# Performance work log

Measured on AMD Instinct MI355X. Metric: run time of the kernel, lower is better.

## Reference

```python
import jax, jax.numpy as jnp
import numpy as np

N = 4096
IN_F = 256
OUT_F = 128
H = 2
ALPHA = 0.2  # leaky relu slope
NEG_INF = -9e15  # matches -9000000000000000.0 in the torch code


def setup_inputs() -> dict:
    key = jax.random.key(0)
    k_x, k_adj, k_w, k_a = jax.random.split(key, 4)
    x = jax.random.normal(k_x, (N, IN_F), dtype=jnp.float32)
    adj = (jax.random.uniform(k_adj, (N, N)) < 0.005).astype(jnp.float32)
    # xavier_uniform with gain=1.414 as in the torch module
    gain = 1.414
    bound_w = gain * np.sqrt(6.0 / (IN_F + OUT_F))
    W = jax.random.uniform(k_w, (H, IN_F, OUT_F), minval=-bound_w, maxval=bound_w, dtype=jnp.float32)
    bound_a = gain * np.sqrt(6.0 / (2 * OUT_F + 1))
    a = jax.random.uniform(k_a, (H, 2 * OUT_F, 1), minval=-bound_a, maxval=bound_a, dtype=jnp.float32)
    return {"x": x, "adj": adj, "W": W, "a": a}


def reference(x, adj, W, a):
    # Dense multi-head GAT layer (eval mode: dropout is identity).
    n = x.shape[0]
    h, _, f_out = W.shape
    adj = adj + jnp.eye(n, dtype=adj.dtype)  # add self loops
    xt = jnp.einsum('nf,hfo->hno', x, W)  # [H, N, F_out]
    # The repeat_interleave/repeat + concat + matmul(a) in the original is
    # exactly the additive decomposition: score[h,i,j] = xt[h,i]@a1[h] + xt[h,j]@a2[h]
    a1 = a[:, :f_out, 0]   # [H, F_out] (applied to target/query node i)
    a2 = a[:, f_out:, 0]   # [H, F_out] (applied to source node j)
    e1 = jnp.einsum('hno,ho->hn', xt, a1)  # [H, N]
    e2 = jnp.einsum('hno,ho->hn', xt, a2)  # [H, N]
    scores = jax.nn.leaky_relu(e1[:, :, None] + e2[:, None, :], negative_slope=ALPHA)  # [H,N,N]
    scores = jnp.where(adj > 0, scores, jnp.asarray(NEG_INF, scores.dtype))
    attn = jax.nn.softmax(scores, axis=-1)
    h_prime = jnp.einsum('hij,hjo->hio', attn, xt)  # [H, N, F_out]
    # concat=True branch: torch .view(N, H*F_out) on contiguous [H,N,F] -> same as reshape
    return jax.nn.elu(h_prime.reshape(n, h * f_out))
```

## Files before the change

### kernel.cpp

```cpp
#include <hip/hip_runtime.h>
#include <math.h>

#define IN_F 256
#define OUT_F 128
#define NHEAD 2
#define ALPHA 0.2f
#define NN 4096
#define NCAP 128

typedef __attribute__((ext_vector_type(8))) short short8;
typedef __attribute__((ext_vector_type(4))) float f32x4;
typedef const __attribute__((address_space(1))) void* gas_ptr;
typedef __attribute__((address_space(3))) void* las_ptr;

__device__ __forceinline__ void async_copy16(const void* g, void* l) {
  __builtin_amdgcn_global_load_lds((gas_ptr)g, (las_ptr)l, 16, 0, 0);
}

__device__ __forceinline__ ushort f2bf(float f) {
  unsigned u = __float_as_uint(f);
  u += 0x7fffu + ((u >> 16) & 1u);
  return (ushort)(u >> 16);
}

__device__ __forceinline__ float lrelu(float t) { return t > 0.f ? t : ALPHA * t; }

__global__ __launch_bounds__(256) void prep_w(
    const float* __restrict__ W, ushort* __restrict__ Wt) {
  int p = blockIdx.x * 256 + threadIdx.x;
  int h = p >> 13;
  int rem = p & 8191;
  int c = rem >> 7;
  int o = rem & 127;
  const float* wsrc = W + h * (IN_F * OUT_F) + (4 * c) * OUT_F + o;
  ushort4 ov;
  ov.x = f2bf(wsrc[0 * OUT_F]);
  ov.y = f2bf(wsrc[1 * OUT_F]);
  ov.z = f2bf(wsrc[2 * OUT_F]);
  ov.w = f2bf(wsrc[3 * OUT_F]);
  *(ushort4*)(Wt + ((size_t)h * OUT_F + o) * IN_F + 4 * c) = ov;
}

__global__ __launch_bounds__(256) void gemm_mfma(
    const float* __restrict__ x, const ushort* __restrict__ Wt,
    const float* __restrict__ a,
    float* __restrict__ xt, float* __restrict__ e1, float* __restrict__ e2) {
  __shared__ ushort sA[32 * 256];
  __shared__ ushort sB[128 * 256];
  __shared__ float sa[2 * OUT_F];
  __shared__ float se1[32], se2[32];

  const int h = blockIdx.y;
  const int rowBase = blockIdx.x * 32;
  const int tid = threadIdx.x;
  const int wave = tid >> 6, lane = tid & 63;
  const int wr = wave & 1, wc = wave >> 1;
  const int q = lane >> 4, l16 = lane & 15;
  const int ar = tid >> 3;
  const int ak = (tid & 7) * 8;

  const char* wbase = (const char*)(Wt + (size_t)h * (OUT_F * IN_F));
#pragma unroll
  for (int it = 0; it < 16; ++it) {
    int g = it * 256 + tid;
    int r = g >> 5, c32 = g & 31;
    async_copy16(wbase + r * 512 + ((c32 ^ (r & 7)) * 16),
                 (char*)sB + (size_t)(it * 256 + wave * 64) * 16);
  }

  const float* xrow = x + (size_t)(rowBase + ar) * IN_F + ak;
  float4 ax[8];
#pragma unroll
  for (int c = 0; c < 4; ++c) {
    ax[2 * c]     = *(const float4*)(xrow + 64 * c);
    ax[2 * c + 1] = *(const float4*)(xrow + 64 * c + 4);
  }
#pragma unroll
  for (int c = 0; c < 4; ++c) {
    float4 va = ax[2 * c], vb = ax[2 * c + 1];
    union { short8 s8; ushort u[8]; } pk;
    pk.u[0] = f2bf(va.x); pk.u[1] = f2bf(va.y);
    pk.u[2] = f2bf(va.z); pk.u[3] = f2bf(va.w);
    pk.u[4] = f2bf(vb.x); pk.u[5] = f2bf(vb.y);
    pk.u[6] = f2bf(vb.z); pk.u[7] = f2bf(vb.w);
    *(short8*)(sA + ar * 256 + ((ak + 64 * c) ^ ((ar & 7) << 3))) = pk.s8;
  }

  sa[tid] = a[h * (2 * OUT_F) + tid];

  f32x4 acc[4];
#pragma unroll
  for (int i = 0; i < 4; ++i) acc[i] = (f32x4)(0.0f);

  __syncthreads();

  const int arow = wr * 16 + l16;
  const int aswz = (arow & 7) << 3;
#pragma unroll
  for (int ks = 0; ks < 256; ks += 32) {
    short8 af = *(const short8*)(sA + arow * 256 + ((ks + q * 8) ^ aswz));
#pragma unroll
    for (int ct = 0; ct < 4; ++ct) {
      int col = wc * 64 + ct * 16 + l16;
      short8 bf = *(const short8*)(sB + col * 256 + ((ks + q * 8) ^ ((col & 7) << 3)));
      acc[ct] = __builtin_amdgcn_mfma_f32_16x16x32_bf16(af, bf, acc[ct], 0, 0, 0);
    }
  }

#pragma unroll
  for (int ct = 0; ct < 4; ++ct) {
    int col = wc * 64 + ct * 16 + l16;
#pragma unroll
    for (int reg = 0; reg < 4; ++reg) {
      int row = rowBase + wr * 16 + q * 4 + reg;
      xt[((size_t)h * NN + row) * OUT_F + col] = acc[ct][reg];
    }
  }

  float pe1[4], pe2[4];
#pragma unroll
  for (int reg = 0; reg < 4; ++reg) { pe1[reg] = 0.f; pe2[reg] = 0.f; }
#pragma unroll
  for (int ct = 0; ct < 4; ++ct) {
    int col = wc * 64 + ct * 16 + l16;
    float a1v = sa[col], a2v = sa[OUT_F + col];
#pragma unroll
    for (int reg = 0; reg < 4; ++reg) {
      pe1[reg] = fmaf(acc[ct][reg], a1v, pe1[reg]);
      pe2[reg] = fmaf(acc[ct][reg], a2v, pe2[reg]);
    }
  }
#pragma unroll
  for (int off = 1; off < 16; off <<= 1) {
#pragma unroll
    for (int reg = 0; reg < 4; ++reg) {
      pe1[reg] += __shfl_xor(pe1[reg], off, 64);
      pe2[reg] += __shfl_xor(pe2[reg], off, 64);
    }
  }
  if (wc == 0 && l16 == 0) {
#pragma unroll
    for (int reg = 0; reg < 4; ++reg) {
      int r = wr * 16 + q * 4 + reg;
      se1[r] = pe1[reg];
      se2[r] = pe2[reg];
    }
  }
  __syncthreads();
  if (wc == 1 && l16 == 0) {
#pragma unroll
    for (int reg = 0; reg < 4; ++reg) {
      int r = wr * 16 + q * 4 + reg;
      se1[r] += pe1[reg];
      se2[r] += pe2[reg];
    }
  }
  __syncthreads();
  if (tid < 32) {
    e1[(size_t)h * NN + rowBase + tid] = se1[tid];
    e2[(size_t)h * NN + rowBase + tid] = se2[tid];
  }
}

__global__ __launch_bounds__(256) void gat_aggregate(
    const float* __restrict__ adj, const float* __restrict__ xt,
    const float* __restrict__ e1, const float* __restrict__ e2,
    float* __restrict__ out) {
  __shared__ int s_nbr[4][NCAP];
  __shared__ float s_p0[4][NCAP];
  __shared__ float s_p1[4][NCAP];

  const int wave = threadIdx.x >> 6;
  const int lane = threadIdx.x & 63;
  const int i = blockIdx.x * 4 + wave;

  const float4* row4 = (const float4*)(adj + (size_t)i * NN);
  float4 v[16];
#pragma unroll
  for (int c = 0; c < 16; ++c) v[c] = row4[lane + c * 64];

  const unsigned long long lt = (1ull << lane) - 1ull;
  int cnt = 0;
#pragma unroll
  for (int c = 0; c < 16; ++c) {
    float vals[4] = {v[c].x, v[c].y, v[c].z, v[c].w};
#pragma unroll
    for (int s = 0; s < 4; ++s) {
      int j = (c * 64 + lane) * 4 + s;
      bool hit = (vals[s] > 0.f) || (j == i);
      unsigned long long mask = __ballot(hit);
      if (hit) {
        int pos = cnt + (int)__popcll(mask & lt);
        if (pos < NCAP) s_nbr[wave][pos] = j;
      }
      cnt += (int)__popcll(mask);
    }
  }
  const int m = cnt < NCAP ? cnt : NCAP;

  const float e10 = e1[i];
  const float e11 = e1[NN + i];
  float t0[2], t1[2];
  float mx0 = -3.0e38f, mx1 = -3.0e38f;
#pragma unroll
  for (int r = 0; r < 2; ++r) {
    int k = lane + r * 64;
    if (k < m) {
      int j = s_nbr[wave][k];
      t0[r] = lrelu(e10 + e2[j]);
      t1[r] = lrelu(e11 + e2[NN + j]);
      mx0 = fmaxf(mx0, t0[r]);
      mx1 = fmaxf(mx1, t1[r]);
    } else {
      t0[r] = -3.0e38f;
      t1[r] = -3.0e38f;
    }
  }
#pragma unroll
  for (int off = 32; off > 0; off >>= 1) {
    mx0 = fmaxf(mx0, __shfl_xor(mx0, off, 64));
    mx1 = fmaxf(mx1, __shfl_xor(mx1, off, 64));
  }

  float s0 = 0.f, s1 = 0.f;
#pragma unroll
  for (int r = 0; r < 2; ++r) {
    int k = lane + r * 64;
    if (k < m) {
      float p0 = __expf(t0[r] - mx0);
      float p1 = __expf(t1[r] - mx1);
      s_p0[wave][k] = p0;
      s_p1[wave][k] = p1;
      s0 += p0;
      s1 += p1;
    }
  }
#pragma unroll
  for (int off = 32; off > 0; off >>= 1) {
    s0 += __shfl_xor(s0, off, 64);
    s1 += __shfl_xor(s1, off, 64);
  }

  const int h = lane >> 5;
  const int o4 = (lane & 31) * 4;
  const float linv = 1.0f / (h ? s1 : s0);
  const float* pw = h ? s_p1[wave] : s_p0[wave];
  const int* nb = s_nbr[wave];
  const float* xth = xt + (size_t)h * NN * OUT_F + o4;

  f32x4 acc = (f32x4)(0.0f);
  int k = 0;
  for (; k + 4 <= m; k += 4) {
    int j0 = nb[k], j1 = nb[k + 1], j2 = nb[k + 2], j3 = nb[k + 3];
    float w0 = pw[k], w1 = pw[k + 1], w2 = pw[k + 2], w3 = pw[k + 3];
    f32x4 x0 = *(const f32x4*)(xth + (size_t)j0 * OUT_F);
    f32x4 x1 = *(const f32x4*)(xth + (size_t)j1 * OUT_F);
    f32x4 x2 = *(const f32x4*)(xth + (size_t)j2 * OUT_F);
    f32x4 x3 = *(const f32x4*)(xth + (size_t)j3 * OUT_F);
    acc += w0 * x0;
    acc += w1 * x1;
    acc += w2 * x2;
    acc += w3 * x3;
  }
  for (; k < m; ++k) {
    f32x4 xv = *(const f32x4*)(xth + (size_t)nb[k] * OUT_F);
    acc += pw[k] * xv;
  }

  f32x4 r;
#pragma unroll
  for (int e = 0; e < 4; ++e) {
    float av = acc[e] * linv;
    r[e] = av > 0.f ? av : (__expf(av) - 1.0f);
  }
  *(f32x4*)(out + ((size_t)h * NN + i) * OUT_F + o4) = r;
}

extern "C" void kernel_launch(void* const* d_in, const int* in_sizes, int n_in,
                              void* d_out, int out_size, void* d_ws, size_t ws_size,
                              hipStream_t stream) {
  const float* x   = (const float*)d_in[0];
  const float* adj = (const float*)d_in[1];
  const float* W   = (const float*)d_in[2];
  const float* a   = (const float*)d_in[3];
  float* out = (float*)d_out;

  float* xt = (float*)d_ws;
  float* e1 = xt + (size_t)NHEAD * NN * OUT_F;
  float* e2 = e1 + (size_t)NHEAD * NN;
  ushort* Wt = (ushort*)(e2 + (size_t)NHEAD * NN);

  prep_w<<<64, 256, 0, stream>>>(W, Wt);
  gemm_mfma<<<dim3(NN / 32, NHEAD), 256, 0, stream>>>(x, Wt, a, xt, e1, e2);
  gat_aggregate<<<NN / 4, 256, 0, stream>>>(adj, xt, e1, e2, out);
}
```

Before: 112.3 us.

## Fuse weight prep, GEMM and aggregation into one cooperative kernel with grid syncs

Replaces three kernel launches with a single cooperative kernel of 256 blocks that uses grid.sync between the weight conversion, the projection GEMM and the attention aggregation phases. The adjacency scan for the block's 16 rows is done before the GEMM sync, so its global reads can overlap the GEMM phase. This removes launch gaps but runs the aggregation with only 256 blocks, each looping over 4 rows per wave, and raises LDS use per block, which may limit occupancy.

```diff
diff --git a/kernel.cpp b/kernel.cpp
--- a/kernel.cpp
+++ b/kernel.cpp
@@ -1,5 +1,8 @@
 #include <hip/hip_runtime.h>
+#include <hip/hip_cooperative_groups.h>
 #include <math.h>
+
+namespace cg = cooperative_groups;
 
 #define IN_F 256
 #define OUT_F 128
@@ -7,6 +10,7 @@
 #define ALPHA 0.2f
 #define NN 4096
 #define NCAP 128
+#define RPB 16
 
 typedef __attribute__((ext_vector_type(8))) short short8;
 typedef __attribute__((ext_vector_type(4))) float f32x4;
@@ -25,35 +29,42 @@
 
 __device__ __forceinline__ float lrelu(float t) { return t > 0.f ? t : ALPHA * t; }
 
-__global__ __launch_bounds__(256) void prep_w(
-    const float* __restrict__ W, ushort* __restrict__ Wt) {
-  int p = blockIdx.x * 256 + threadIdx.x;
-  int h = p >> 13;
-  int rem = p & 8191;
-  int c = rem >> 7;
-  int o = rem & 127;
-  const float* wsrc = W + h * (IN_F * OUT_F) + (4 * c) * OUT_F + o;
-  ushort4 ov;
-  ov.x = f2bf(wsrc[0 * OUT_F]);
-  ov.y = f2bf(wsrc[1 * OUT_F]);
-  ov.z = f2bf(wsrc[2 * OUT_F]);
-  ov.w = f2bf(wsrc[3 * OUT_F]);
-  *(ushort4*)(Wt + ((size_t)h * OUT_F + o) * IN_F + 4 * c) = ov;
-}
-
-__global__ __launch_bounds__(256) void gemm_mfma(
-    const float* __restrict__ x, const ushort* __restrict__ Wt,
-    const float* __restrict__ a,
-    float* __restrict__ xt, float* __restrict__ e1, float* __restrict__ e2) {
+__global__ __launch_bounds__(256, 2) void gat_fused(
+    const float* __restrict__ x, const float* __restrict__ adj,
+    const float* __restrict__ W, const float* __restrict__ a_,
+    ushort* __restrict__ Wt, float* __restrict__ xt,
+    float* __restrict__ e1, float* __restrict__ e2,
+    float* __restrict__ out) {
   __shared__ ushort sA[32 * 256];
   __shared__ ushort sB[128 * 256];
   __shared__ float sa[2 * OUT_F];
   __shared__ float se1[32], se2[32];
-
-  const int h = blockIdx.y;
-  const int rowBase = blockIdx.x * 32;
+  __shared__ int   s_nbr[RPB][NCAP];
+  __shared__ float s_p0[RPB][NCAP];
+  __shared__ float s_p1[RPB][NCAP];
+
+  cg::grid_group grid = cg::this_grid();
+
+  const int bid = blockIdx.x;
   const int tid = threadIdx.x;
   const int wave = tid >> 6, lane = tid & 63;
+
+  if (tid < 64) {
+    int p = bid * 64 + tid;
+    int h0 = p >> 13, rem = p & 8191, c = rem >> 7, o = rem & 127;
+    const float* wsrc = W + h0 * (IN_F * OUT_F) + (4 * c) * OUT_F + o;
+    ushort4 ov;
+    ov.x = f2bf(wsrc[0 * OUT_F]);
+    ov.y = f2bf(wsrc[1 * OUT_F]);
+    ov.z = f2bf(wsrc[2 * OUT_F]);
+    ov.w = f2bf(wsrc[3 * OUT_F]);
+    *(ushort4*)(Wt + ((size_t)h0 * OUT_F + o) * IN_F + 4 * c) = ov;
+  }
+
+  grid.sync();
+
+  const int h = bid >> 7;
+  const int rowBase = (bid & 127) * 32;
   const int wr = wave & 1, wc = wave >> 1;
   const int q = lane >> 4, l16 = lane & 15;
   const int ar = tid >> 3;
@@ -69,15 +80,15 @@
   }
 
   const float* xrow = x + (size_t)(rowBase + ar) * IN_F + ak;
-  float4 ax[8];
+  float4 axv[8];
 #pragma unroll
   for (int c = 0; c < 4; ++c) {
-    ax[2 * c]     = *(const float4*)(xrow + 64 * c);
-    ax[2 * c + 1] = *(const float4*)(xrow + 64 * c + 4);
+    axv[2 * c]     = *(const float4*)(xrow + 64 * c);
+    axv[2 * c + 1] = *(const float4*)(xrow + 64 * c + 4);
   }
 #pragma unroll
   for (int c = 0; c < 4; ++c) {
-    float4 va = ax[2 * c], vb = ax[2 * c + 1];
+    float4 va = axv[2 * c], vb = axv[2 * c + 1];
     union { short8 s8; ushort u[8]; } pk;
     pk.u[0] = f2bf(va.x); pk.u[1] = f2bf(va.y);
     pk.u[2] = f2bf(va.z); pk.u[3] = f2bf(va.w);
@@ -85,12 +96,40 @@
     pk.u[6] = f2bf(vb.z); pk.u[7] = f2bf(vb.w);
     *(short8*)(sA + ar * 256 + ((ak + 64 * c) ^ ((ar & 7) << 3))) = pk.s8;
   }
-
-  sa[tid] = a[h * (2 * OUT_F) + tid];
+  sa[tid] = a_[h * (2 * OUT_F) + tid];
+
+  int m_r[4];
+  const unsigned long long lt = (1ull << lane) - 1ull;
+#pragma unroll
+  for (int rr = 0; rr < 4; ++rr) {
+    const int widx = wave * 4 + rr;
+    const int i = bid * RPB + widx;
+    const float4* row4 = (const float4*)(adj + (size_t)i * NN);
+    float4 v[16];
+#pragma unroll
+    for (int c = 0; c < 16; ++c) v[c] = row4[lane + c * 64];
+    int total = 0;
+#pragma unroll
+    for (int c = 0; c < 16; ++c) {
+      float vals[4] = {v[c].x, v[c].y, v[c].z, v[c].w};
+#pragma unroll
+      for (int s = 0; s < 4; ++s) {
+        int j = (c * 64 + lane) * 4 + s;
+        bool hit = (vals[s] > 0.f) || (j == i);
+        unsigned long long mask = __ballot(hit);
+        if (hit) {
+          int pos = total + (int)__popcll(mask & lt);
+          if (pos < NCAP) s_nbr[widx][pos] = j;
+        }
+        total += (int)__popcll(mask);
+      }
+    }
+    m_r[rr] = total < NCAP ? total : NCAP;
+  }
 
   f32x4 acc[4];
 #pragma unroll
-  for (int i = 0; i < 4; ++i) acc[i] = (f32x4)(0.0f);
+  for (int i2 = 0; i2 < 4; ++i2) acc[i2] = (f32x4)(0.0f);
 
   __syncthreads();
 
@@ -160,120 +199,92 @@
     e1[(size_t)h * NN + rowBase + tid] = se1[tid];
     e2[(size_t)h * NN + rowBase + tid] = se2[tid];
   }
-}
-
-__global__ __launch_bounds__(256) void gat_aggregate(
-    const float* __restrict__ adj, const float* __restrict__ xt,
-    const float* __restrict__ e1, const float* __restrict__ e2,
-    float* __restrict__ out) {
-  __shared__ int s_nbr[4][NCAP];
-  __shared__ float s_p0[4][NCAP];
-  __shared__ float s_p1[4][NCAP];
-
-  const int wave = threadIdx.x >> 6;
-  const int lane = threadIdx.x & 63;
-  const int i = blockIdx.x * 4 + wave;
-
-  const float4* row4 = (const float4*)(adj + (size_t)i * NN);
-  float4 v[16];
-#pragma unroll
-  for (int c = 0; c < 16; ++c) v[c] = row4[lane + c * 64];
-
-  const unsigned long long lt = (1ull << lane) - 1ull;
-  int cnt = 0;
-#pragma unroll
-  for (int c = 0; c < 16; ++c) {
-    float vals[4] = {v[c].x, v[c].y, v[c].z, v[c].w};
-#pragma unroll
-    for (int s = 0; s < 4; ++s) {
-      int j = (c * 64 + lane) * 4 + s;
-      bool hit = (vals[s] > 0.f) || (j == i);
-      unsigned long long mask = __ballot(hit);
-      if (hit) {
-        int pos = cnt + (int)__popcll(mask & lt);
-        if (pos < NCAP) s_nbr[wave][pos] = j;
+
+  grid.sync();
+
+  const int h2 = lane >> 5;
+  const int o4 = (lane & 31) * 4;
+#pragma unroll
+  for (int rr = 0; rr < 4; ++rr) {
+    const int widx = wave * 4 + rr;
+    const int i = bid * RPB + widx;
+    const int m = m_r[rr];
+
+    const float e10 = e1[i];
+    const float e11 = e1[NN + i];
+    float t0[2], t1[2];
+    float mx0 = -3.0e38f, mx1 = -3.0e38f;
+#pragma unroll
+    for (int r = 0; r < 2; ++r) {
+      int k = lane + r * 64;
+      if (k < m) {
+        int j = s_nbr[widx][k];
+        t0[r] = lrelu(e10 + e2[j]);
+        t1[r] = lrelu(e11 + e2[NN + j]);
+        mx0 = fmaxf(mx0, t0[r]);
+        mx1 = fmaxf(mx1, t1[r]);
+      } else {
+        t0[r] = -3.0e38f;
+        t1[r] = -3.0e38f;
       }
-      cnt += (int)__popcll(mask);
-    }
-  }
-  const int m = cnt < NCAP ? cnt : NCAP;
-
-  const float e10 = e1[i];
-  const float e11 = e1[NN + i];
-  float t0[2], t1[2];
-  float mx0 = -3.0e38f, mx1 = -3.0e38f;
-#pragma unroll
-  for (int r = 0; r < 2; ++r) {
-    int k = lane + r * 64;
-    if (k < m) {
-      int j = s_nbr[wave][k];
-      t0[r] = lrelu(e10 + e2[j]);
-      t1[r] = lrelu(e11 + e2[NN + j]);
-      mx0 = fmaxf(mx0, t0[r]);
-      mx1 = fmaxf(mx1, t1[r]);
-    } else {
-      t0[r] = -3.0e38f;
-      t1[r] = -3.0e38f;
-    }
-  }
-#pragma unroll
-  for (int off = 32; off > 0; off >>= 1) {
-    mx0 = fmaxf(mx0, __shfl_xor(mx0, off, 64));
-    mx1 = fmaxf(mx1, __shfl_xor(mx1, off, 64));
-  }
-
-  float s0 = 0.f, s1 = 0.f;
-#pragma unroll
-  for (int r = 0; r < 2; ++r) {
-    int k = lane + r * 64;
-    if (k < m) {
-      float p0 = __expf(t0[r] - mx0);
-      float p1 = __expf(t1[r] - mx1);
-      s_p0[wave][k] = p0;
-      s_p1[wave][k] = p1;
-      s0 += p0;
-      s1 += p1;
-    }
-  }
-#pragma unroll
-  for (int off = 32; off > 0; off >>= 1) {
-    s0 += __shfl_xor(s0, off, 64);
-    s1 += __shfl_xor(s1, off, 64);
-  }
-
-  const int h = lane >> 5;
-  const int o4 = (lane & 31) * 4;
-  const float linv = 1.0f / (h ? s1 : s0);
-  const float* pw = h ? s_p1[wave] : s_p0[wave];
-  const int* nb = s_nbr[wave];
-  const float* xth = xt + (size_t)h * NN * OUT_F + o4;
-
-  f32x4 acc = (f32x4)(0.0f);
-  int k = 0;
-  for (; k + 4 <= m; k += 4) {
-    int j0 = nb[k], j1 = nb[k + 1], j2 = nb[k + 2], j3 = nb[k + 3];
-    float w0 = pw[k], w1 = pw[k + 1], w2 = pw[k + 2], w3 = pw[k + 3];
-    f32x4 x0 = *(const f32x4*)(xth + (size_t)j0 * OUT_F);
-    f32x4 x1 = *(const f32x4*)(xth + (size_t)j1 * OUT_F);
-    f32x4 x2 = *(const f32x4*)(xth + (size_t)j2 * OUT_F);
-    f32x4 x3 = *(const f32x4*)(xth + (size_t)j3 * OUT_F);
-    acc += w0 * x0;
-    acc += w1 * x1;
-    acc += w2 * x2;
-    acc += w3 * x3;
-  }
-  for (; k < m; ++k) {
-    f32x4 xv = *(const f32x4*)(xth + (size_t)nb[k] * OUT_F);
-    acc += pw[k] * xv;
-  }
-
-  f32x4 r;
-#pragma unroll
-  for (int e = 0; e < 4; ++e) {
-    float av = acc[e] * linv;
-    r[e] = av > 0.f ? av : (__expf(av) - 1.0f);
-  }
-  *(f32x4*)(out + ((size_t)h * NN + i) * OUT_F + o4) = r;
+    }
+#pragma unroll
+    for (int off = 32; off > 0; off >>= 1) {
+      mx0 = fmaxf(mx0, __shfl_xor(mx0, off, 64));
+      mx1 = fmaxf(mx1, __shfl_xor(mx1, off, 64));
+    }
+
+    float s0 = 0.f, s1 = 0.f;
+#pragma unroll
+    for (int r = 0; r < 2; ++r) {
+      int k = lane + r * 64;
+      if (k < m) {
+        float p0 = __expf(t0[r] - mx0);
+        float p1 = __expf(t1[r] - mx1);
+        s_p0[widx][k] = p0;
+        s_p1[widx][k] = p1;
+        s0 += p0;
+        s1 += p1;
+      }
+    }
+#pragma unroll
+    for (int off = 32; off > 0; off >>= 1) {
+      s0 += __shfl_xor(s0, off, 64);
+      s1 += __shfl_xor(s1, off, 64);
+    }
+
+    const float linv = 1.0f / (h2 ? s1 : s0);
+    const float* pw = h2 ? s_p1[widx] : s_p0[widx];
+    const int* nb = s_nbr[widx];
+    const float* xth = xt + (size_t)h2 * NN * OUT_F + o4;
+
+    f32x4 accv = (f32x4)(0.0f);
+    int k = 0;
+    for (; k + 4 <= m; k += 4) {
+      int j0 = nb[k], j1 = nb[k + 1], j2 = nb[k + 2], j3 = nb[k + 3];
+      float w0 = pw[k], w1 = pw[k + 1], w2 = pw[k + 2], w3 = pw[k + 3];
+      f32x4 x0 = *(const f32x4*)(xth + (size_t)j0 * OUT_F);
+      f32x4 x1 = *(const f32x4*)(xth + (size_t)j1 * OUT_F);
+      f32x4 x2 = *(const f32x4*)(xth + (size_t)j2 * OUT_F);
+      f32x4 x3 = *(const f32x4*)(xth + (size_t)j3 * OUT_F);
+      accv += w0 * x0;
+      accv += w1 * x1;
+      accv += w2 * x2;
+      accv += w3 * x3;
+    }
+    for (; k < m; ++k) {
+      f32x4 xv = *(const f32x4*)(xth + (size_t)nb[k] * OUT_F);
+      accv += pw[k] * xv;
+    }
+
+    f32x4 r;
+#pragma unroll
+    for (int e = 0; e < 4; ++e) {
+      float av = accv[e] * linv;
+      r[e] = av > 0.f ? av : (__expf(av) - 1.0f);
+    }
+    *(f32x4*)(out + ((size_t)h2 * NN + i) * OUT_F + o4) = r;
+  }
 }
 
 extern "C" void kernel_launch(void* const* d_in, const int* in_sizes, int n_in,
@@ -290,7 +301,8 @@
   float* e2 = e1 + (size_t)NHEAD * NN;
   ushort* Wt = (ushort*)(e2 + (size_t)NHEAD * NN);
 
-  prep_w<<<64, 256, 0, stream>>>(W, Wt);
-  gemm_mfma<<<dim3(NN / 32, NHEAD), 256, 0, stream>>>(x, Wt, a, xt, e1, e2);
-  gat_aggregate<<<NN / 4, 256, 0, stream>>>(adj, xt, e1, e2, out);
+  void* args[] = {(void*)&x, (void*)&adj, (void*)&W, (void*)&a,
+                  (void*)&Wt, (void*)&xt, (void*)&e1, (void*)&e2, (void*)&out};
+  hipLaunchCooperativeKernel((const void*)gat_fused, dim3(256), dim3(256),
+                             args, 0, stream);
 }
```

Result: slower. 192.3 us (+71.3%).
